# Kernel tuning notes

Measured on AMD Instinct MI355X. Metric: run time of the kernel, lower is better.

Reference implementation:

```python
import jax, jax.numpy as jnp
import numpy as np

EPS = 1e-6        # module eps added to softplus(sigma)
BALL_EPS = 1e-5   # clip margin for Poincare ball projection


def _norm(x):
    return jnp.sqrt(jnp.clip(jnp.sum(x * x, axis=-1, keepdims=True), 1e-15))


def _clip_norm(x, max_norm):
    n = _norm(x)
    return x * jnp.minimum(1.0, max_norm / n)


def _artanh(x):
    return jnp.arctanh(jnp.clip(x, -1.0 + 1e-7, 1.0 - 1e-7))


def _expmap0(u, c):
    """pre_clip -> PoincareBall.expmap0 -> post_clip."""
    sc = jnp.sqrt(c)
    max_tan = jnp.arctanh(jnp.asarray(1.0 - BALL_EPS, u.dtype)) / sc
    u = _clip_norm(u, max_tan)                      # pre_clip on tangent norm
    n = _norm(u)
    y = jnp.tanh(sc * n) * u / (sc * n)
    return _clip_norm(y, (1.0 - BALL_EPS) / sc)     # post_clip inside ball


def _logmap0(y, c):
    sc = jnp.sqrt(c)
    n = _norm(y)
    return _artanh(sc * n) * y / (sc * n)


def _pair_dist(qh, kh, c):
    """Poincare distance d(q_i, k_j) computed from inner products (no [B,H,N,J,D] tensor).
    qh: (B,H,N,D), kh: (B,H,J,D) -> (B,H,N,J).
    d = (2/sqrt(c)) * artanh(sqrt(c) * ||(-q) mobius_add k||).
    """
    x2 = jnp.sum(qh * qh, -1)[..., :, None]   # (B,H,N,1)
    y2 = jnp.sum(kh * kh, -1)[..., None, :]   # (B,H,1,J)
    xy = jnp.einsum('bhnd,bhjd->bhnj', qh, kh)
    A = 1.0 - 2.0 * c * xy + c * y2
    Bc = 1.0 - c * x2
    num2 = A * A * x2 - 2.0 * A * Bc * xy + Bc * Bc * y2   # ||numerator||^2
    den = 1.0 - 2.0 * c * xy + (c * c) * x2 * y2
    arg = jnp.sqrt(c) * jnp.sqrt(jnp.clip(num2, 0.0)) / jnp.clip(den, 1e-15)
    return (2.0 / jnp.sqrt(c)) * _artanh(arg)


def _mobius_scalar_mul(r, x, c):
    sc = jnp.sqrt(c)
    n = _norm(x)
    return jnp.tanh(r * _artanh(sc * n)) * x / (sc * n)


def setup_inputs() -> dict:
    key = jax.random.key(0)
    ks = jax.random.split(key, 8)
    B, N, D, H, M = 16, 576, 768, 12, 128
    Hd = D // H
    std = 0.02
    isp1 = float(np.log(np.expm1(1.0)))  # inv_softplus(1.0)
    return {
        'x': jax.random.normal(ks[0], (B, N, D), jnp.float32),
        'Wq': jax.random.normal(ks[1], (D, D), jnp.float32) * std,
        'bq': jnp.zeros((D,), jnp.float32),
        'Wk': jax.random.normal(ks[2], (D, D), jnp.float32) * std,
        'bk': jnp.zeros((D,), jnp.float32),
        'Wv': jax.random.normal(ks[3], (D, D), jnp.float32) * std,
        'bv': jnp.zeros((D,), jnp.float32),
        'Wo': jax.random.normal(ks[4], (D, D), jnp.float32) * std,
        'bo': jnp.zeros((D,), jnp.float32),
        'centroids': jax.random.normal(ks[5], (H, M, Hd), jnp.float32) * std,
        'curv_raw': jnp.full((1,), isp1, jnp.float32),
        'sigma_raw': jnp.full((H,), isp1, jnp.float32),
    }


def reference(x, Wq, bq, Wk, bk, Wv, bv, Wo, bo, centroids, curv_raw, sigma_raw):
    B, N, D = x.shape
    H, M, Hd = centroids.shape
    c = jax.nn.softplus(curv_raw[0])

    def split(t):  # (B,N,D) -> (B,H,N,Hd)
        return t.reshape(B, N, H, Hd).transpose(0, 2, 1, 3)

    q = split(x @ Wq.T + bq)
    k = split(x @ Wk.T + bk)
    v = split(x @ Wv.T + bv)

    Cb = jnp.broadcast_to(centroids[None], (B, H, M, Hd))
    K_aug = jnp.concatenate([k, Cb], axis=2)   # (B,H,J,Hd), J = N + M
    V_aug = jnp.concatenate([v, Cb], axis=2)

    q_h = _expmap0(q, c)
    K_h = _expmap0(K_aug, c)
    V_h = _expmap0(V_aug, c)

    d = _pair_dist(q_h, K_h, c)                              # (B,H,N,J)
    sigma = (jax.nn.softplus(sigma_raw) + EPS)[None, :, None, None]
    W = jax.nn.softmax(-(d * d) / (2.0 * sigma * sigma), axis=-1)

    # Riemannian weighted midpoint (geoopt weighted_midpoint with k=-c):
    # gamma = lambda_x = 2 / (1 - c||x||^2)
    gamma = 2.0 / jnp.clip(1.0 - c * jnp.sum(V_h * V_h, -1), 1e-15)  # (B,H,J)
    nom = jnp.einsum('bhnj,bhjd->bhnd', W * gamma[:, :, None, :], V_h)
    den = jnp.einsum('bhnj,bhj->bhn', W, gamma - 1.0)
    den = jnp.where(den >= 0, jnp.maximum(den, 1e-10), jnp.minimum(den, -1e-10))
    two_mean = nom / den[..., None]
    O_h = _mobius_scalar_mul(0.5, two_mean, c)
    O_euc = _logmap0(O_h, c)                                  # (B,H,N,Hd)

    out = O_euc.transpose(0, 2, 1, 3).reshape(B, N, H * Hd)
    return out @ Wo.T + bo
```

## Files before the change

kernel.cpp:

```cpp
#include <hip/hip_runtime.h>
#include <cstdint>
#include <cstddef>

#define B_  16
#define N_  576
#define D_  768
#define H_  12
#define HD_ 64
#define M_  128
#define J_  704

typedef unsigned short u16;
typedef __attribute__((ext_vector_type(8))) short bf16x8;
typedef __attribute__((ext_vector_type(4))) float f32x4;
typedef __attribute__((ext_vector_type(4))) unsigned short u16x4;
typedef __attribute__((ext_vector_type(8))) unsigned short u16x8;


__device__ __forceinline__ float softplus_f(float x) {
    return (x > 20.f) ? x : log1pf(expf(x));
}

__device__ __forceinline__ float wred_sum64(float v) {
#pragma unroll
    for (int m = 1; m < 64; m <<= 1) v += __shfl_xor(v, m, 64);
    return v;
}

__device__ __forceinline__ u16 bf16_rne(float f) {
    unsigned int u = __float_as_uint(f);
    unsigned int r = u + 0x7FFFu + ((u >> 16) & 1u);
    return (u16)(r >> 16);
}
__device__ __forceinline__ float bf16_tof(u16 h) {
    return __uint_as_float(((unsigned int)h) << 16);
}

__device__ __forceinline__ float expmap0_factor(float n2, float sc, float* n2out) {
    const float ATANH_1M1E5 = 6.1030335f;
    float n0 = sqrtf(fmaxf(n2, 1e-15f));
    float maxtan = ATANH_1M1E5 / sc;
    float f1 = fminf(1.f, maxtan / n0);
    float n1 = n0 * f1;
    float a  = sc * n1;
    float th = tanhf(a);
    float yfac  = th / a;
    float ynorm = th / sc;
    float lim   = (1.f - 1e-5f) / sc;
    float f2 = fminf(1.f, lim / ynorm);
    float fn = ynorm * f2;
    *n2out = fn * fn;
    return f1 * yfac * f2;
}

__device__ __forceinline__ float artanh_fast(float z) {
    return 0.5f * __logf((1.f + z) / (1.f - z));
}

typedef const __attribute__((address_space(1))) unsigned int* gas_u32;
typedef __attribute__((address_space(3))) unsigned int* las_u32;
__device__ __forceinline__ void gload_lds16(const u16* g, u16* l) {
    __builtin_amdgcn_global_load_lds((gas_u32)(const void*)g, (las_u32)(void*)l, 16, 0, 0);
}

__global__ __launch_bounds__(256) void split_bf16_kernel(
    const float* __restrict__ src, u16* __restrict__ hi, u16* __restrict__ lo, int n4)
{
    int i = blockIdx.x * 256 + threadIdx.x;
    if (i >= n4) return;
    float4 v = ((const float4*)src)[i];
    u16x4 h, l;
    h[0] = bf16_rne(v.x); l[0] = bf16_rne(v.x - bf16_tof(h[0]));
    h[1] = bf16_rne(v.y); l[1] = bf16_rne(v.y - bf16_tof(h[1]));
    h[2] = bf16_rne(v.z); l[2] = bf16_rne(v.z - bf16_tof(h[2]));
    h[3] = bf16_rne(v.w); l[3] = bf16_rne(v.w - bf16_tof(h[3]));
    ((u16x4*)hi)[i] = h;
    ((u16x4*)lo)[i] = l;
}

__global__ __launch_bounds__(256) void split_w4_kernel(
    const float* __restrict__ W0, const float* __restrict__ W1,
    const float* __restrict__ W2, const float* __restrict__ W3,
    u16* __restrict__ H0, u16* __restrict__ L0, u16* __restrict__ H1, u16* __restrict__ L1,
    u16* __restrict__ H2, u16* __restrict__ L2, u16* __restrict__ H3, u16* __restrict__ L3)
{
    int i = blockIdx.x * 256 + threadIdx.x;
    const int wsel = blockIdx.y;
    const float* src = wsel == 0 ? W0 : (wsel == 1 ? W1 : (wsel == 2 ? W2 : W3));
    u16* hi = wsel == 0 ? H0 : (wsel == 1 ? H1 : (wsel == 2 ? H2 : H3));
    u16* lo = wsel == 0 ? L0 : (wsel == 1 ? L1 : (wsel == 2 ? L2 : L3));
    float4 v = ((const float4*)src)[i];
    u16x4 h, l;
    h[0] = bf16_rne(v.x); l[0] = bf16_rne(v.x - bf16_tof(h[0]));
    h[1] = bf16_rne(v.y); l[1] = bf16_rne(v.y - bf16_tof(h[1]));
    h[2] = bf16_rne(v.z); l[2] = bf16_rne(v.z - bf16_tof(h[2]));
    h[3] = bf16_rne(v.w); l[3] = bf16_rne(v.w - bf16_tof(h[3]));
    ((u16x4*)hi)[i] = h;
    ((u16x4*)lo)[i] = l;
}

__global__ __launch_bounds__(256) void gemm_qkv_mfma(
    const u16* __restrict__ xh, const u16* __restrict__ xl,
    const u16* __restrict__ Wh0, const u16* __restrict__ Wl0,
    const u16* __restrict__ Wh1, const u16* __restrict__ Wl1,
    const u16* __restrict__ Wh2, const u16* __restrict__ Wl2,
    const float* __restrict__ bq, const float* __restrict__ bk, const float* __restrict__ bv,
    u16* __restrict__ Qb0, u16* __restrict__ Qb1, u16* __restrict__ Qb2,
    u16* __restrict__ Kb0, u16* __restrict__ Kb1, u16* __restrict__ Kb2,
    u16* __restrict__ gV0, u16* __restrict__ gV1,
    float* __restrict__ x2q, float* __restrict__ y2g, float* __restrict__ gm1,
    float* __restrict__ rbj,
    const float* __restrict__ curv_raw)
{
    __shared__ u16 Ah[4096], Al[4096], Bh[4096], Bl[4096];
    const int tid = threadIdx.x;
    const int w = tid >> 6, lane = tid & 63;
    const int wr = w >> 1, wc = w & 1;
    const int lrow = lane & 15, lk8 = (lane >> 4) << 3;
    const int bid = blockIdx.x;
    const int xcd = bid & 7, ser = bid >> 3;
    const int mt = xcd * 9 + (ser % 9);
    const int yb = ser / 9;
    const int which = yb / 6, ct = yb - which * 6;
    const u16* Bp_h = which == 0 ? Wh0 : (which == 1 ? Wh1 : Wh2);
    const u16* Bp_l = which == 0 ? Wl0 : (which == 1 ? Wl1 : Wl2);
    const int row0 = mt * 128, col0 = ct * 128;

    const size_t a0 = (size_t)(row0 + (2 * w + 0) * 16 + lrow) * 768 + lk8;
    const size_t a1 = a0 + 16 * 768;
    const size_t b0 = (size_t)(col0 + (2 * w + 0) * 16 + lrow) * 768 + lk8;
    const size_t b1 = b0 + 16 * 768;
    u16* lAh0 = Ah + (2 * w) * 512; u16* lAh1 = lAh0 + 512;
    u16* lAl0 = Al + (2 * w) * 512; u16* lAl1 = lAl0 + 512;
    u16* lBh0 = Bh + (2 * w) * 512; u16* lBh1 = lBh0 + 512;
    u16* lBl0 = Bl + (2 * w) * 512; u16* lBl1 = lBl0 + 512;

    f32x4 acc[4][4];
#pragma unroll
    for (int i = 0; i < 4; ++i)
#pragma unroll
        for (int j = 0; j < 4; ++j) acc[i][j] = (f32x4){0.f, 0.f, 0.f, 0.f};

    for (int k0 = 0; k0 < 768; k0 += 32) {
        gload_lds16(xh + a0 + k0, lAh0);
        gload_lds16(xh + a1 + k0, lAh1);
        gload_lds16(xl + a0 + k0, lAl0);
        gload_lds16(xl + a1 + k0, lAl1);
        gload_lds16(Bp_h + b0 + k0, lBh0);
        gload_lds16(Bp_h + b1 + k0, lBh1);
        gload_lds16(Bp_l + b0 + k0, lBl0);
        gload_lds16(Bp_l + b1 + k0, lBl1);
        __syncthreads();
        bf16x8 aH[4], aL[4], bH[4], bL[4];
        const int lo8 = lane * 8;
#pragma unroll
        for (int i = 0; i < 4; ++i) {
            aH[i] = *(const bf16x8*)(Ah + (wr * 4 + i) * 512 + lo8);
            aL[i] = *(const bf16x8*)(Al + (wr * 4 + i) * 512 + lo8);
            bH[i] = *(const bf16x8*)(Bh + (wc * 4 + i) * 512 + lo8);
            bL[i] = *(const bf16x8*)(Bl + (wc * 4 + i) * 512 + lo8);
        }
#pragma unroll
        for (int mi = 0; mi < 4; ++mi)
#pragma unroll
            for (int ni = 0; ni < 4; ++ni) {
                acc[mi][ni] = __builtin_amdgcn_mfma_f32_16x16x32_bf16(aH[mi], bH[ni], acc[mi][ni], 0, 0, 0);
                acc[mi][ni] = __builtin_amdgcn_mfma_f32_16x16x32_bf16(aH[mi], bL[ni], acc[mi][ni], 0, 0, 0);
                acc[mi][ni] = __builtin_amdgcn_mfma_f32_16x16x32_bf16(aL[mi], bH[ni], acc[mi][ni], 0, 0, 0);
            }
        __syncthreads();
    }

    const float* bias = which == 0 ? bq : (which == 1 ? bk : bv);
    const int h = ct * 2 + wc;
    const int rbase = row0 + wr * 64 + ((lane >> 4) << 2);
    const float c  = softplus_f(curv_raw[0]);
    const float sc = sqrtf(c);
    float bvv[4];
#pragma unroll
    for (int ni = 0; ni < 4; ++ni) bvv[ni] = bias[h * 64 + ni * 16 + lrow];

#pragma unroll
    for (int mi = 0; mi < 4; ++mi) {
        float v4[4][4];
#pragma unroll
        for (int ni = 0; ni < 4; ++ni) {
            f32x4 a = acc[mi][ni];
#pragma unroll
            for (int r = 0; r < 4; ++r) v4[ni][r] = a[r] + bvv[ni];
        }
        float f_[4], n2o_[4];
#pragma unroll
        for (int r = 0; r < 4; ++r) {
            float p[4];
#pragma unroll
            for (int ni = 0; ni < 4; ++ni) {
                float s = v4[ni][r] * v4[ni][r];
#pragma unroll
                for (int m = 1; m < 16; m <<= 1) s += __shfl_xor(s, m, 64);
                p[ni] = s;
            }
            float n2 = (p[0] + p[1]) + (p[2] + p[3]);
            f_[r] = expmap0_factor(n2, sc, &n2o_[r]);
        }
        const int row0g = rbase + mi * 16;
        const int bb = row0g / 576;
        const int nn0 = row0g - bb * 576;
        const size_t gbase = ((size_t)(bb * 12 + h)) * 576 + nn0;
        if (which == 2) {
            float gmm[4];
#pragma unroll
            for (int r = 0; r < 4; ++r) gmm[r] = 2.f / fmaxf(1.f - c * n2o_[r], 1e-15f);
            if (lrow == 0) {
#pragma unroll
                for (int r = 0; r < 4; ++r) gm1[gbase + r] = gmm[r] - 1.f;
            }
#pragma unroll
            for (int ni = 0; ni < 4; ++ni) {
                const int hd = ni * 16 + lrow;
                u16x4 hs, ls;
#pragma unroll
                for (int r = 0; r < 4; ++r) {
                    float gv = v4[ni][r] * f_[r] * gmm[r];
                    u16 hb = bf16_rne(gv);
                    hs[r] = hb;
                    ls[r] = bf16_rne(gv - bf16_tof(hb));
                }
                const size_t dst = (((size_t)(bb * 12 + h)) * 64 + hd) * 576 + nn0;
                *(u16x4*)(gV0 + dst) = hs;
                *(u16x4*)(gV1 + dst) = ls;
            }
        } else {
            float* scal = which == 0 ? x2q : y2g;
            if (lrow == 0) {
#pragma unroll
                for (int r = 0; r < 4; ++r) scal[gbase + r] = n2o_[r];
                if (which == 1) {
#pragma unroll
                    for (int r = 0; r < 4; ++r)
                        rbj[gbase + r] = 1.f / fmaf(-c, n2o_[r], 1.f);
                }
            }
            u16* P0 = which == 0 ? Qb0 : Kb0;
            u16* P1 = which == 0 ? Qb1 : Kb1;
            u16* P2 = which == 0 ? Qb2 : Kb2;
#pragma unroll
            for (int ni = 0; ni < 4; ++ni) {
                const int hd = ni * 16 + lrow;
#pragma unroll
                for (int r = 0; r < 4; ++r) {
                    float y = v4[ni][r] * f_[r];
                    u16 hb = bf16_rne(y);
                    float r1 = y - bf16_tof(hb);
                    u16 mb = bf16_rne(r1);
                    u16 lb = bf16_rne(r1 - bf16_tof(mb));
                    const size_t off = (gbase + r) * 64 + hd;
                    P0[off] = hb; P1[off] = mb; P2[off] = lb;
                }
            }
        }
    }
}

__global__ __launch_bounds__(256) void gemm_o_mfma(
    const u16* __restrict__ Oh, const u16* __restrict__ Ol,
    const u16* __restrict__ Wh, const u16* __restrict__ Wl,
    const float* __restrict__ bo, float* __restrict__ out)
{
    __shared__ u16 Ah[4096], Al[4096], Bh[4096], Bl[4096];
    const int tid = threadIdx.x;
    const int w = tid >> 6, lane = tid & 63;
    const int wr = w >> 1, wc = w & 1;
    const int lrow = lane & 15, lk8 = (lane >> 4) << 3;
    const int bid = blockIdx.x;
    const int xcd = bid & 7, ser = bid >> 3;
    const int mt = xcd * 9 + (ser % 9);
    const int ct = ser / 9;
    const int row0 = mt * 128, col0 = ct * 128;

    const size_t a0 = (size_t)(row0 + (2 * w + 0) * 16 + lrow) * 768 + lk8;
    const size_t a1 = a0 + 16 * 768;
    const size_t b0 = (size_t)(col0 + (2 * w + 0) * 16 + lrow) * 768 + lk8;
    const size_t b1 = b0 + 16 * 768;
    u16* lAh0 = Ah + (2 * w) * 512; u16* lAh1 = lAh0 + 512;
    u16* lAl0 = Al + (2 * w) * 512; u16* lAl1 = lAl0 + 512;
    u16* lBh0 = Bh + (2 * w) * 512; u16* lBh1 = lBh0 + 512;
    u16* lBl0 = Bl + (2 * w) * 512; u16* lBl1 = lBl0 + 512;

    f32x4 acc[4][4];
#pragma unroll
    for (int i = 0; i < 4; ++i)
#pragma unroll
        for (int j = 0; j < 4; ++j) acc[i][j] = (f32x4){0.f, 0.f, 0.f, 0.f};

    for (int k0 = 0; k0 < 768; k0 += 32) {
        gload_lds16(Oh + a0 + k0, lAh0);
        gload_lds16(Oh + a1 + k0, lAh1);
        gload_lds16(Ol + a0 + k0, lAl0);
        gload_lds16(Ol + a1 + k0, lAl1);
        gload_lds16(Wh + b0 + k0, lBh0);
        gload_lds16(Wh + b1 + k0, lBh1);
        gload_lds16(Wl + b0 + k0, lBl0);
        gload_lds16(Wl + b1 + k0, lBl1);
        __syncthreads();
        bf16x8 aH[4], aL[4], bH[4], bL[4];
        const int lo8 = lane * 8;
#pragma unroll
        for (int i = 0; i < 4; ++i) {
            aH[i] = *(const bf16x8*)(Ah + (wr * 4 + i) * 512 + lo8);
            aL[i] = *(const bf16x8*)(Al + (wr * 4 + i) * 512 + lo8);
            bH[i] = *(const bf16x8*)(Bh + (wc * 4 + i) * 512 + lo8);
            bL[i] = *(const bf16x8*)(Bl + (wc * 4 + i) * 512 + lo8);
        }
#pragma unroll
        for (int mi = 0; mi < 4; ++mi)
#pragma unroll
            for (int ni = 0; ni < 4; ++ni) {
                acc[mi][ni] = __builtin_amdgcn_mfma_f32_16x16x32_bf16(aH[mi], bH[ni], acc[mi][ni], 0, 0, 0);
                acc[mi][ni] = __builtin_amdgcn_mfma_f32_16x16x32_bf16(aH[mi], bL[ni], acc[mi][ni], 0, 0, 0);
                acc[mi][ni] = __builtin_amdgcn_mfma_f32_16x16x32_bf16(aL[mi], bH[ni], acc[mi][ni], 0, 0, 0);
            }
        __syncthreads();
    }

    const int rbase = row0 + wr * 64 + ((lane >> 4) << 2);
#pragma unroll
    for (int ni = 0; ni < 4; ++ni) {
        const int colg = col0 + wc * 64 + ni * 16 + lrow;
        const float bv_ = bo[colg];
#pragma unroll
        for (int mi = 0; mi < 4; ++mi) {
            f32x4 a = acc[mi][ni];
#pragma unroll
            for (int r = 0; r < 4; ++r) {
                int row = rbase + mi * 16 + r;
                out[(size_t)row * 768 + colg] = a[r] + bv_;
            }
        }
    }
}

__global__ __launch_bounds__(256) void cent_kernel(
    const float* __restrict__ cent,
    u16* __restrict__ Kc0, u16* __restrict__ Kc1, u16* __restrict__ Kc2,
    u16* __restrict__ gVc0, u16* __restrict__ gVc1,
    float* __restrict__ y2c, float* __restrict__ gm1c, float* __restrict__ rbc,
    const float* __restrict__ curv_raw)
{
    __shared__ float gvt_s[64][65];
    const float c  = softplus_f(curv_raw[0]);
    const float sc = sqrtf(c);
    const int t = blockIdx.x;
    const int h = t >> 1, ct = t & 1;
    const int w = threadIdx.x >> 6, lane = threadIdx.x & 63;
#pragma unroll 4
    for (int i = 0; i < 16; ++i) {
        const int m = ct * 64 + w * 16 + i;
        const size_t g = (size_t)h * 128 + m;
        float cv = cent[g * 64 + lane];
        float n2 = wred_sum64(cv * cv);
        float n2o;
        float f = expmap0_factor(n2, sc, &n2o);
        float ky = cv * f;
        u16 kh = bf16_rne(ky);
        float r1 = ky - bf16_tof(kh);
        u16 km = bf16_rne(r1);
        u16 kl = bf16_rne(r1 - bf16_tof(km));
        Kc0[g * 64 + lane] = kh; Kc1[g * 64 + lane] = km; Kc2[g * 64 + lane] = kl;
        float gmm = 2.f / fmaxf(1.f - c * n2o, 1e-15f);
        gvt_s[lane][w * 16 + i] = ky * gmm;
        if (lane == 0) {
            y2c[g] = n2o; gm1c[g] = gmm - 1.f;
            rbc[g] = 1.f / fmaf(-c, n2o, 1.f);
        }
    }
    __syncthreads();
    const int hd = threadIdx.x >> 2, j0 = (threadIdx.x & 3) * 16;
    u16 hb[16], lb[16];
#pragma unroll
    for (int e = 0; e < 16; ++e) {
        float v = gvt_s[hd][j0 + e];
        hb[e] = bf16_rne(v);
        lb[e] = bf16_rne(v - bf16_tof(hb[e]));
    }
    const size_t dst = ((size_t)h * 64 + hd) * 128 + ct * 64 + j0;
    *(u16x8*)(gVc0 + dst)     = *(u16x8*)&hb[0];
    *(u16x8*)(gVc0 + dst + 8) = *(u16x8*)&hb[8];
    *(u16x8*)(gVc1 + dst)     = *(u16x8*)&lb[0];
    *(u16x8*)(gVc1 + dst + 8) = *(u16x8*)&lb[8];
}

__global__ __launch_bounds__(256) void attn_kernel(
    const u16* __restrict__ Qb0, const u16* __restrict__ Qb1, const u16* __restrict__ Qb2,
    const u16* __restrict__ Kb0, const u16* __restrict__ Kb1, const u16* __restrict__ Kb2,
    const u16* __restrict__ Kc0, const u16* __restrict__ Kc1, const u16* __restrict__ Kc2,
    const u16* __restrict__ gV0, const u16* __restrict__ gV1,
    const u16* __restrict__ gVc0, const u16* __restrict__ gVc1,
    const float* __restrict__ x2q, const float* __restrict__ y2g, const float* __restrict__ gm1,
    const float* __restrict__ y2c, const float* __restrict__ gm1c,
    const float* __restrict__ rbj, const float* __restrict__ rbc,
    const float* __restrict__ sigma_raw, const float* __restrict__ curv_raw,
    u16* __restrict__ Oh, u16* __restrict__ Ol)
{
    __shared__ __align__(16) u16 Kst[2][3][4096];
    __shared__ __align__(16) u16 Vst[2][4096];
    __shared__ __align__(16) u16 wb_hi[4][1024];
    __shared__ __align__(16) u16 wb_lo[4][1024];

    const int blk = blockIdx.x;
    const int xcd = blk & 7;
    const int serial = blk >> 3;
    const int bhg = serial / 9;
    const int qt = serial - bhg * 9;
    const int bh = bhg * 8 + xcd;
    const int b = bh / 12, h = bh % 12;
    const float c  = softplus_f(curv_raw[0]);
    const float sc = sqrtf(c);
    const float sig = softplus_f(sigma_raw[h]) + 1e-6f;
    const float coef = -2.f / (c * sig * sig);
    const float c2h  = coef * 0.25f * 0.6931471805599453f;

    const int tid = threadIdx.x;
    const int w = tid >> 6, lane = tid & 63;
    const int lr = lane & 15, lg = lane >> 4, lo8 = lg * 8;
    const int swl = (lr & 7) << 3;

    const size_t qbase = (size_t)bh * 576 + qt * 64;

    int srow[2], scol[2];
#pragma unroll
    for (int rr = 0; rr < 2; ++rr) {
        int cch = (rr * 4 + w) * 64 + lane;
        srow[rr] = cch >> 3;
        scol[rr] = ((cch & 7) ^ (srow[rr] & 7)) << 3;
    }
    const size_t kb_base = (size_t)bh * 576 * 64;
    const size_t kc_base = (size_t)h * 128 * 64;
    const size_t vb_base = (size_t)bh * 64 * 576;
    const size_t vc_base = (size_t)h * 64 * 128;

    auto stageK = [&](int t, int buf) {
        if (t < 9) {
            const size_t rb = kb_base + (size_t)t * 64 * 64;
#pragma unroll
            for (int rr = 0; rr < 2; ++rr) {
                const size_t so = rb + (size_t)srow[rr] * 64 + scol[rr];
                gload_lds16(Kb0 + so, &Kst[buf][0][(rr * 4 + w) * 512]);
                gload_lds16(Kb1 + so, &Kst[buf][1][(rr * 4 + w) * 512]);
                gload_lds16(Kb2 + so, &Kst[buf][2][(rr * 4 + w) * 512]);
            }
        } else {
            const size_t rb = kc_base + (size_t)(t - 9) * 64 * 64;
#pragma unroll
            for (int rr = 0; rr < 2; ++rr) {
                const size_t so = rb + (size_t)srow[rr] * 64 + scol[rr];
                gload_lds16(Kc0 + so, &Kst[buf][0][(rr * 4 + w) * 512]);
                gload_lds16(Kc1 + so, &Kst[buf][1][(rr * 4 + w) * 512]);
                gload_lds16(Kc2 + so, &Kst[buf][2][(rr * 4 + w) * 512]);
            }
        }
    };
    auto stageV = [&](int t) {
        if (t < 9) {
            const size_t rb = vb_base + (size_t)t * 64;
#pragma unroll
            for (int rr = 0; rr < 2; ++rr) {
                const size_t so = rb + (size_t)srow[rr] * 576 + scol[rr];
                gload_lds16(gV0 + so, &Vst[0][(rr * 4 + w) * 512]);
                gload_lds16(gV1 + so, &Vst[1][(rr * 4 + w) * 512]);
            }
        } else {
            const size_t rb = vc_base + (size_t)(t - 9) * 64;
#pragma unroll
            for (int rr = 0; rr < 2; ++rr) {
                const size_t so = rb + (size_t)srow[rr] * 128 + scol[rr];
                gload_lds16(gVc0 + so, &Vst[0][(rr * 4 + w) * 512]);
                gload_lds16(gVc1 + so, &Vst[1][(rr * 4 + w) * 512]);
            }
        }
    };

    bf16x8 aQh[2], aQm[2], aQl[2];
    {
        const size_t qrow = (qbase + w * 16 + lr) * 64;
#pragma unroll
        for (int kt = 0; kt < 2; ++kt) {
            const size_t o = qrow + kt * 32 + lo8;
            aQh[kt] = *(const bf16x8*)(Qb0 + o);
            aQm[kt] = *(const bf16x8*)(Qb1 + o);
            aQl[kt] = *(const bf16x8*)(Qb2 + o);
        }
    }
    float x2r[4], Pr[4];
#pragma unroll
    for (int r = 0; r < 4; ++r) {
        float x2 = x2q[qbase + w * 16 + lg * 4 + r];
        x2r[r] = x2;
        Pr[r] = (c + c) / fmaf(-c, x2, 1.f);
    }

    f32x4 pv[4];
#pragma unroll
    for (int i = 0; i < 4; ++i) pv[i] = (f32x4){0.f, 0.f, 0.f, 0.f};
    float den[4] = {0.f, 0.f, 0.f, 0.f};

    u16* wbh = &wb_hi[w][0];
    u16* wbl = &wb_lo[w][0];

    stageK(0, 0);
    __syncthreads();

    int cur = 0;
    for (int jt = 0; jt < 11; ++jt) {
        const int jb = jt * 64;

        if (jt < 10) stageK(jt + 1, cur ^ 1);
        stageV(jt);

        const float* y2p;
        const float* gm1p;
        const float* rbp;
        if (jt < 9) {
            y2p = y2g + (size_t)bh * 576 + jb;  gm1p = gm1 + (size_t)bh * 576 + jb;
            rbp = rbj + (size_t)bh * 576 + jb;
        } else {
            y2p = y2c + (size_t)h * 128 + (jb - 576); gm1p = gm1c + (size_t)h * 128 + (jb - 576);
            rbp = rbc + (size_t)h * 128 + (jb - 576);
        }

        const u16* kp0 = &Kst[cur][0][0];
        const u16* kp1 = &Kst[cur][1][0];
        const u16* kp2 = &Kst[cur][2][0];
        f32x4 sf[4];
        float y2v[4], gm1v[4], rbv[4];
#pragma unroll
        for (int jf = 0; jf < 4; ++jf) {
            y2v[jf] = y2p[jf * 16 + lr];
            gm1v[jf] = gm1p[jf * 16 + lr];
            rbv[jf] = rbp[jf * 16 + lr];
            const int rb = (jf * 16 + lr) * 64;
            f32x4 s = (f32x4){0.f, 0.f, 0.f, 0.f};
#pragma unroll
            for (int kt = 0; kt < 2; ++kt) {
                const int o = rb + ((kt * 32 + lo8) ^ swl);
                bf16x8 kh = *(const bf16x8*)(kp0 + o);
                bf16x8 km = *(const bf16x8*)(kp1 + o);
                bf16x8 kl = *(const bf16x8*)(kp2 + o);
                s = __builtin_amdgcn_mfma_f32_16x16x32_bf16(aQh[kt], kh, s, 0, 0, 0);
                s = __builtin_amdgcn_mfma_f32_16x16x32_bf16(aQh[kt], km, s, 0, 0, 0);
                s = __builtin_amdgcn_mfma_f32_16x16x32_bf16(aQm[kt], kh, s, 0, 0, 0);
                s = __builtin_amdgcn_mfma_f32_16x16x32_bf16(aQm[kt], km, s, 0, 0, 0);
                s = __builtin_amdgcn_mfma_f32_16x16x32_bf16(aQh[kt], kl, s, 0, 0, 0);
                s = __builtin_amdgcn_mfma_f32_16x16x32_bf16(aQl[kt], kh, s, 0, 0, 0);
            }
            sf[jf] = s;
        }

#pragma unroll
        for (int jf = 0; jf < 4; ++jf) {
            const float y2 = y2v[jf];
            const float rb_ = rbv[jf];
#pragma unroll
            for (int r = 0; r < 4; ++r) {
                float xy = sf[jf][r];
                float sxy = x2r[r] + y2;
                float u = fmaf(-2.f, xy, sxy);
                float krr = Pr[r] * rb_;
                float z = fmaxf(fmaf(krr, u, 1.f), 1.f);
                float zm = fmaxf(fmaf(z, z, -1.f), 0.f);
                float lg = __builtin_amdgcn_logf(z + __builtin_amdgcn_sqrtf(zm));
                float wv_ = __builtin_amdgcn_exp2f(c2h * (lg * lg));
                sf[jf][r] = wv_;
                den[r] = fmaf(wv_, gm1v[jf], den[r]);
            }
        }

#pragma unroll
        for (int r = 0; r < 4; ++r) {
            const int row = lg * 4 + r;
            const int sw = (row & 7) << 3;
#pragma unroll
            for (int jf = 0; jf < 4; ++jf) {
                const int colu = (jf * 16 + lr) ^ sw;
                float wv_ = sf[jf][r];
                u16 hb = bf16_rne(wv_);
                wbh[row * 64 + colu] = hb;
                wbl[row * 64 + colu] = bf16_rne(wv_ - bf16_tof(hb));
            }
        }

        __syncthreads();

        bf16x8 aWh[2], aWl[2];
#pragma unroll
        for (int kt = 0; kt < 2; ++kt) {
            const int colu = (kt * 32 + lo8) ^ swl;
            aWh[kt] = *(const bf16x8*)(wbh + lr * 64 + colu);
            aWl[kt] = *(const bf16x8*)(wbl + lr * 64 + colu);
        }

#pragma unroll
        for (int hf = 0; hf < 4; ++hf) {
            const int rb = (hf * 16 + lr) * 64;
#pragma unroll
            for (int kt = 0; kt < 2; ++kt) {
                const int o = rb + ((kt * 32 + lo8) ^ swl);
                bf16x8 vh = *(const bf16x8*)(&Vst[0][o]);
                bf16x8 vl = *(const bf16x8*)(&Vst[1][o]);
                pv[hf] = __builtin_amdgcn_mfma_f32_16x16x32_bf16(aWh[kt], vh, pv[hf], 0, 0, 0);
                pv[hf] = __builtin_amdgcn_mfma_f32_16x16x32_bf16(aWh[kt], vl, pv[hf], 0, 0, 0);
                pv[hf] = __builtin_amdgcn_mfma_f32_16x16x32_bf16(aWl[kt], vh, pv[hf], 0, 0, 0);
            }
        }

        __syncthreads();
        cur ^= 1;
    }

#pragma unroll
    for (int r = 0; r < 4; ++r) {
        float d = den[r];
#pragma unroll
        for (int msk = 1; msk < 16; msk <<= 1) d += __shfl_xor(d, msk, 64);
        float rd = 1.f / d;
        float o_[4];
        float n2 = 0.f;
#pragma unroll
        for (int hf = 0; hf < 4; ++hf) { o_[hf] = pv[hf][r] * rd; n2 = fmaf(o_[hf], o_[hf], n2); }
#pragma unroll
        for (int msk = 1; msk < 16; msk <<= 1) n2 += __shfl_xor(n2, msk, 64);
        float nrm = sqrtf(fmaxf(n2, 1e-15f));
        float arg = fminf(sc * nrm, 1.f - 1e-7f);
        float t = artanh_fast(arg);
        float f = 0.5f * t / (sc * nrm);
        const int nrow = qt * 64 + w * 16 + lg * 4 + r;
        const size_t dst = ((size_t)(b * 576 + nrow)) * 768 + h * 64;
#pragma unroll
        for (int hf = 0; hf < 4; ++hf) {
            float val = o_[hf] * f;
            u16 hb = bf16_rne(val);
            Oh[dst + hf * 16 + lr] = hb;
            Ol[dst + hf * 16 + lr] = bf16_rne(val - bf16_tof(hb));
        }
    }
}

extern "C" void kernel_launch(void* const* d_in, const int* in_sizes, int n_in,
                              void* d_out, int out_size, void* d_ws, size_t ws_size,
                              hipStream_t stream) {
    (void)in_sizes; (void)n_in; (void)out_size; (void)ws_size;
    const float* x    = (const float*)d_in[0];
    const float* Wq   = (const float*)d_in[1];
    const float* bq   = (const float*)d_in[2];
    const float* Wk   = (const float*)d_in[3];
    const float* bk   = (const float*)d_in[4];
    const float* Wv   = (const float*)d_in[5];
    const float* bv   = (const float*)d_in[6];
    const float* Wo   = (const float*)d_in[7];
    const float* bo   = (const float*)d_in[8];
    const float* cent = (const float*)d_in[9];
    const float* curv = (const float*)d_in[10];
    const float* sigr = (const float*)d_in[11];
    float* out = (float*)d_out;

    const size_t QH  = (size_t)B_ * H_ * N_ * 64;
    const size_t CK  = (size_t)H_ * M_ * 64;
    const size_t WSZ = (size_t)D_ * D_;

    float* fp = (float*)d_ws;
    float* x2q  = fp;            fp += (size_t)B_ * H_ * N_;
    float* y2g  = fp;            fp += (size_t)B_ * H_ * N_;
    float* gm1  = fp;            fp += (size_t)B_ * H_ * N_;
    float* rbjv = fp;            fp += (size_t)B_ * H_ * N_;
    float* y2c  = fp;            fp += (size_t)H_ * M_;
    float* gm1c = fp;            fp += (size_t)H_ * M_;
    float* rbcv = fp;            fp += (size_t)H_ * M_;
    u16* up = (u16*)fp;
    u16* xh  = up;  up += QH;
    u16* xl  = up;  up += QH;
    u16* Oh  = xh;
    u16* Ol  = xl;
    u16* Wqh = up;  up += WSZ;
    u16* Wql = up;  up += WSZ;
    u16* Wkh = up;  up += WSZ;
    u16* Wkl = up;  up += WSZ;
    u16* Wvh = up;  up += WSZ;
    u16* Wvl = up;  up += WSZ;
    u16* Woh = up;  up += WSZ;
    u16* Wol = up;  up += WSZ;
    u16* Qb  = up;  up += 3 * QH;
    u16* Kb  = up;  up += 3 * QH;
    u16* gV  = up;  up += 2 * QH;
    u16* Kc  = up;  up += 3 * CK;
    u16* gVc = up;  up += 2 * CK;

    u16* Qb0 = Qb;           u16* Qb1 = Qb + QH;   u16* Qb2 = Qb + 2 * QH;
    u16* Kb0 = Kb;           u16* Kb1 = Kb + QH;   u16* Kb2 = Kb + 2 * QH;
    u16* gV0 = gV;           u16* gV1 = gV + QH;
    u16* Kc0 = Kc;           u16* Kc1 = Kc + CK;   u16* Kc2 = Kc + 2 * CK;
    u16* gVc0 = gVc;         u16* gVc1 = gVc + CK;

    split_bf16_kernel<<<(int)(QH / 4 / 256), 256, 0, stream>>>(x, xh, xl, (int)(QH / 4));
    split_w4_kernel<<<dim3((int)(WSZ / 4 / 256), 4), 256, 0, stream>>>(
        Wq, Wk, Wv, Wo, Wqh, Wql, Wkh, Wkl, Wvh, Wvl, Woh, Wol);

    cent_kernel<<<24, 256, 0, stream>>>(cent, Kc0, Kc1, Kc2, gVc0, gVc1, y2c, gm1c, rbcv, curv);

    gemm_qkv_mfma<<<1296, 256, 0, stream>>>(xh, xl, Wqh, Wql, Wkh, Wkl, Wvh, Wvl,
                                            bq, bk, bv,
                                            Qb0, Qb1, Qb2, Kb0, Kb1, Kb2, gV0, gV1,
                                            x2q, y2g, gm1, rbjv, curv);
    attn_kernel<<<1728, 256, 0, stream>>>(Qb0, Qb1, Qb2, Kb0, Kb1, Kb2, Kc0, Kc1, Kc2,
                                          gV0, gV1, gVc0, gVc1,
                                          x2q, y2g, gm1, y2c, gm1c, rbjv, rbcv,
                                          sigr, curv, Oh, Ol);
    gemm_o_mfma<<<432, 256, 0, stream>>>(Oh, Ol, Woh, Wol, bo, out);
}
```

Measured before the change: 392.1 us.

## Prefetch next K-tile during MFMA in projection GEMMs and use fast math intrinsics

Both projection GEMM kernels now issue the global-to-LDS loads for the next K slice right after the current slice has been read into registers. Those loads run while the MFMAs execute, instead of waiting on a barrier before every compute step. The expmap0 factor, gamma and reciprocal computations switch to hardware rcp, sqrt and exp2 intrinsics in place of IEEE division and tanhf. The row-norm reduction is merged into a single shuffle tree. The intrinsics lower accuracy slightly, and the tanh formula via exp2 may lose precision for small arguments.

```diff
diff --git a/kernel.cpp b/kernel.cpp
--- a/kernel.cpp
+++ b/kernel.cpp
@@ -38,17 +38,17 @@
 
 __device__ __forceinline__ float expmap0_factor(float n2, float sc, float* n2out) {
     const float ATANH_1M1E5 = 6.1030335f;
-    float n0 = sqrtf(fmaxf(n2, 1e-15f));
-    float maxtan = ATANH_1M1E5 / sc;
-    float f1 = fminf(1.f, maxtan / n0);
+    const float LOG2E2 = 2.8853900817779268f;
+    float rsc = __builtin_amdgcn_rcpf(sc);
+    float n0 = __builtin_amdgcn_sqrtf(fmaxf(n2, 1e-15f));
+    float f1 = fminf(1.f, (ATANH_1M1E5 * rsc) * __builtin_amdgcn_rcpf(n0));
     float n1 = n0 * f1;
     float a  = sc * n1;
-    float th = tanhf(a);
-    float yfac  = th / a;
-    float ynorm = th / sc;
-    float lim   = (1.f - 1e-5f) / sc;
-    float f2 = fminf(1.f, lim / ynorm);
-    float fn = ynorm * f2;
+    float e2a = __builtin_amdgcn_exp2f(a * LOG2E2);
+    float th  = 1.f - 2.f * __builtin_amdgcn_rcpf(e2a + 1.f);
+    float yfac  = th * __builtin_amdgcn_rcpf(a);
+    float f2 = fminf(1.f, 0.99999f * __builtin_amdgcn_rcpf(th));
+    float fn = (th * rsc) * f2;
     *n2out = fn * fn;
     return f1 * yfac * f2;
 }
@@ -135,13 +135,7 @@
     u16* lBh0 = Bh + (2 * w) * 512; u16* lBh1 = lBh0 + 512;
     u16* lBl0 = Bl + (2 * w) * 512; u16* lBl1 = lBl0 + 512;
 
-    f32x4 acc[4][4];
-#pragma unroll
-    for (int i = 0; i < 4; ++i)
-#pragma unroll
-        for (int j = 0; j < 4; ++j) acc[i][j] = (f32x4){0.f, 0.f, 0.f, 0.f};
-
-    for (int k0 = 0; k0 < 768; k0 += 32) {
+    auto STAGE = [&](int k0) {
         gload_lds16(xh + a0 + k0, lAh0);
         gload_lds16(xh + a1 + k0, lAh1);
         gload_lds16(xl + a0 + k0, lAl0);
@@ -150,9 +144,20 @@
         gload_lds16(Bp_h + b1 + k0, lBh1);
         gload_lds16(Bp_l + b0 + k0, lBl0);
         gload_lds16(Bp_l + b1 + k0, lBl1);
-        __syncthreads();
+    };
+
+    f32x4 acc[4][4];
+#pragma unroll
+    for (int i = 0; i < 4; ++i)
+#pragma unroll
+        for (int j = 0; j < 4; ++j) acc[i][j] = (f32x4){0.f, 0.f, 0.f, 0.f};
+
+    STAGE(0);
+    __syncthreads();
+
+    const int lo8 = lane * 8;
+    for (int k0 = 0; k0 < 768; k0 += 32) {
         bf16x8 aH[4], aL[4], bH[4], bL[4];
-        const int lo8 = lane * 8;
 #pragma unroll
         for (int i = 0; i < 4; ++i) {
             aH[i] = *(const bf16x8*)(Ah + (wr * 4 + i) * 512 + lo8);
@@ -160,6 +165,8 @@
             bH[i] = *(const bf16x8*)(Bh + (wc * 4 + i) * 512 + lo8);
             bL[i] = *(const bf16x8*)(Bl + (wc * 4 + i) * 512 + lo8);
         }
+        __syncthreads();
+        if (k0 < 736) STAGE(k0 + 32);
 #pragma unroll
         for (int mi = 0; mi < 4; ++mi)
 #pragma unroll
@@ -192,16 +199,12 @@
         float f_[4], n2o_[4];
 #pragma unroll
         for (int r = 0; r < 4; ++r) {
-            float p[4];
-#pragma unroll
-            for (int ni = 0; ni < 4; ++ni) {
-                float s = v4[ni][r] * v4[ni][r];
-#pragma unroll
-                for (int m = 1; m < 16; m <<= 1) s += __shfl_xor(s, m, 64);
-                p[ni] = s;
-            }
-            float n2 = (p[0] + p[1]) + (p[2] + p[3]);
-            f_[r] = expmap0_factor(n2, sc, &n2o_[r]);
+            float s = v4[0][r] * v4[0][r];
+#pragma unroll
+            for (int ni = 1; ni < 4; ++ni) s = fmaf(v4[ni][r], v4[ni][r], s);
+#pragma unroll
+            for (int m = 1; m < 16; m <<= 1) s += __shfl_xor(s, m, 64);
+            f_[r] = expmap0_factor(s, sc, &n2o_[r]);
         }
         const int row0g = rbase + mi * 16;
         const int bb = row0g / 576;
@@ -210,7 +213,8 @@
         if (which == 2) {
             float gmm[4];
 #pragma unroll
-            for (int r = 0; r < 4; ++r) gmm[r] = 2.f / fmaxf(1.f - c * n2o_[r], 1e-15f);
+            for (int r = 0; r < 4; ++r)
+                gmm[r] = 2.f * __builtin_amdgcn_rcpf(fmaxf(1.f - c * n2o_[r], 1e-15f));
             if (lrow == 0) {
 #pragma unroll
                 for (int r = 0; r < 4; ++r) gm1[gbase + r] = gmm[r] - 1.f;
@@ -238,7 +242,7 @@
                 if (which == 1) {
 #pragma unroll
                     for (int r = 0; r < 4; ++r)
-                        rbj[gbase + r] = 1.f / fmaf(-c, n2o_[r], 1.f);
+                        rbj[gbase + r] = __builtin_amdgcn_rcpf(fmaf(-c, n2o_[r], 1.f));
                 }
             }
             u16* P0 = which == 0 ? Qb0 : Kb0;
@@ -287,13 +291,7 @@
     u16* lBh0 = Bh + (2 * w) * 512; u16* lBh1 = lBh0 + 512;
     u16* lBl0 = Bl + (2 * w) * 512; u16* lBl1 = lBl0 + 512;
 
-    f32x4 acc[4][4];
-#pragma unroll
-    for (int i = 0; i < 4; ++i)
-#pragma unroll
-        for (int j = 0; j < 4; ++j) acc[i][j] = (f32x4){0.f, 0.f, 0.f, 0.f};
-
-    for (int k0 = 0; k0 < 768; k0 += 32) {
+    auto STAGE = [&](int k0) {
         gload_lds16(Oh + a0 + k0, lAh0);
         gload_lds16(Oh + a1 + k0, lAh1);
         gload_lds16(Ol + a0 + k0, lAl0);
@@ -302,9 +300,20 @@
         gload_lds16(Wh + b1 + k0, lBh1);
         gload_lds16(Wl + b0 + k0, lBl0);
         gload_lds16(Wl + b1 + k0, lBl1);
-        __syncthreads();
+    };
+
+    f32x4 acc[4][4];
+#pragma unroll
+    for (int i = 0; i < 4; ++i)
+#pragma unroll
+        for (int j = 0; j < 4; ++j) acc[i][j] = (f32x4){0.f, 0.f, 0.f, 0.f};
+
+    STAGE(0);
+    __syncthreads();
+
+    const int lo8 = lane * 8;
+    for (int k0 = 0; k0 < 768; k0 += 32) {
         bf16x8 aH[4], aL[4], bH[4], bL[4];
-        const int lo8 = lane * 8;
 #pragma unroll
         for (int i = 0; i < 4; ++i) {
             aH[i] = *(const bf16x8*)(Ah + (wr * 4 + i) * 512 + lo8);
@@ -312,6 +321,8 @@
             bH[i] = *(const bf16x8*)(Bh + (wc * 4 + i) * 512 + lo8);
             bL[i] = *(const bf16x8*)(Bl + (wc * 4 + i) * 512 + lo8);
         }
+        __syncthreads();
+        if (k0 < 736) STAGE(k0 + 32);
 #pragma unroll
         for (int mi = 0; mi < 4; ++mi)
 #pragma unroll
@@ -367,11 +378,11 @@
         u16 km = bf16_rne(r1);
         u16 kl = bf16_rne(r1 - bf16_tof(km));
         Kc0[g * 64 + lane] = kh; Kc1[g * 64 + lane] = km; Kc2[g * 64 + lane] = kl;
-        float gmm = 2.f / fmaxf(1.f - c * n2o, 1e-15f);
+        float gmm = 2.f * __builtin_amdgcn_rcpf(fmaxf(1.f - c * n2o, 1e-15f));
         gvt_s[lane][w * 16 + i] = ky * gmm;
         if (lane == 0) {
             y2c[g] = n2o; gm1c[g] = gmm - 1.f;
-            rbc[g] = 1.f / fmaf(-c, n2o, 1.f);
+            rbc[g] = __builtin_amdgcn_rcpf(fmaf(-c, n2o, 1.f));
         }
     }
     __syncthreads();
```

Measured after the change: 370.5 us. -5.5%, faster.
